# Kernel optimization log

Hardware: AMD Instinct MI355X
Metric: run time of the kernel (lower is better)

## Reference

```python
import jax, jax.numpy as jnp
import numpy as np

D_MODEL = 512
N_HEADS = 4
D_HEAD = D_MODEL // N_HEADS
D_FF = 2048
N_LAYERS = 3
IN_DIM = 25
OUT_DIM = 1
PRE = 20          # pre_training_size
SCALE = 10.0      # scaling_factor
EPS = 1e-5


def setup_inputs() -> dict:
    key = jax.random.key(0)
    ks = jax.random.split(key, 20)
    B, S = 4, 2048
    def gn(k, shape, fan_in):
        return jax.random.normal(k, shape, jnp.float32) * (1.0 / np.sqrt(fan_in))
    return {
        "src": jax.random.normal(ks[0], (B, S, IN_DIM), jnp.float32),
        "emb_w": gn(ks[1], (D_MODEL, IN_DIM), IN_DIM),
        "emb_b": jnp.zeros((D_MODEL,), jnp.float32),
        "in_w": gn(ks[2], (N_LAYERS, 3 * D_MODEL, D_MODEL), D_MODEL),
        "in_b": jnp.zeros((N_LAYERS, 3 * D_MODEL), jnp.float32),
        "out_w": gn(ks[3], (N_LAYERS, D_MODEL, D_MODEL), D_MODEL),
        "out_b": jnp.zeros((N_LAYERS, D_MODEL), jnp.float32),
        "ln1_g": jnp.ones((N_LAYERS, D_MODEL), jnp.float32),
        "ln1_b": jnp.zeros((N_LAYERS, D_MODEL), jnp.float32),
        "ln2_g": jnp.ones((N_LAYERS, D_MODEL), jnp.float32),
        "ln2_b": jnp.zeros((N_LAYERS, D_MODEL), jnp.float32),
        "ff1_w": gn(ks[4], (N_LAYERS, D_FF, D_MODEL), D_MODEL),
        "ff1_b": jnp.zeros((N_LAYERS, D_FF), jnp.float32),
        "ff2_w": gn(ks[5], (N_LAYERS, D_MODEL, D_FF), D_FF),
        "ff2_b": jnp.zeros((N_LAYERS, D_MODEL), jnp.float32),
        "dec_w": gn(ks[6], (OUT_DIM, D_MODEL), D_MODEL),
        "dec_b": jnp.zeros((OUT_DIM,), jnp.float32),
    }


def _layer_norm(x, g, b):
    mu = jnp.mean(x, axis=-1, keepdims=True)
    var = jnp.var(x, axis=-1, keepdims=True)
    return (x - mu) * jax.lax.rsqrt(var + EPS) * g + b


def _pos_encoding(seq_len):
    # eval mode: start index 0, no dropout
    pos = jnp.arange(seq_len, dtype=jnp.float32)[:, None]           # [S,1]
    div = jnp.exp(jnp.arange(0, D_MODEL, 2, dtype=jnp.float32) * (-np.log(10000.0) / D_MODEL))  # [D/2]
    ang = pos * div                                                  # [S,D/2]
    return jnp.stack([jnp.sin(ang), jnp.cos(ang)], axis=-1).reshape(seq_len, D_MODEL)


def _causal_mask(seq_len):
    row = jnp.arange(seq_len)[:, None]
    col = jnp.arange(seq_len)[None, :]
    mask = jnp.where(col <= row, 0.0, -jnp.inf).astype(jnp.float32)
    # include_training_period=True: first PRE x PRE block unmasked
    return mask.at[:PRE, :PRE].set(0.0)


def reference(src, emb_w, emb_b, in_w, in_b, out_w, out_b,
              ln1_g, ln1_b, ln2_g, ln2_b, ff1_w, ff1_b, ff2_w, ff2_b,
              dec_w, dec_b):
    B, S, _ = src.shape
    x = src @ emb_w.T + emb_b                    # [B,S,D]
    x = x + _pos_encoding(S)[None]
    mask = _causal_mask(S)                       # [S,S]
    scale = 1.0 / np.sqrt(D_HEAD)
    for l in range(N_LAYERS):
        # --- self-attention (post-norm, eager bmm+softmax+bmm path) ---
        qkv = x @ in_w[l].T + in_b[l]            # [B,S,3D]
        q, k, v = jnp.split(qkv, 3, axis=-1)
        q = q.reshape(B, S, N_HEADS, D_HEAD).transpose(0, 2, 1, 3)
        k = k.reshape(B, S, N_HEADS, D_HEAD).transpose(0, 2, 1, 3)
        v = v.reshape(B, S, N_HEADS, D_HEAD).transpose(0, 2, 1, 3)
        scores = jnp.einsum('bhqd,bhkd->bhqk', q, k) * scale + mask
        attn = jax.nn.softmax(scores, axis=-1)   # [B,H,S,S] (need_weights=True path)
        o = jnp.einsum('bhqk,bhkd->bhqd', attn, v)
        o = o.transpose(0, 2, 1, 3).reshape(B, S, D_MODEL)
        o = o @ out_w[l].T + out_b[l]
        x = _layer_norm(x + o, ln1_g[l], ln1_b[l])
        # --- FFN ---
        h = jax.nn.relu(x @ ff1_w[l].T + ff1_b[l])
        h = h @ ff2_w[l].T + ff2_b[l]
        x = _layer_norm(x + h, ln2_g[l], ln2_b[l])
    out = jnp.tanh(x @ dec_w.T + dec_b) * SCALE  # [B,S,1]
    return out
```

## Files before the change

kernel.cpp:

```cpp
#include <hip/hip_runtime.h>

#define S_LEN 2048
#define DMODEL 512

typedef __attribute__((ext_vector_type(8))) short bf16x8;
typedef __attribute__((ext_vector_type(4))) float f32x4;
typedef __attribute__((ext_vector_type(4))) unsigned short u16x4;
typedef __attribute__((ext_vector_type(8))) unsigned short u16x8;
typedef __attribute__((ext_vector_type(2))) unsigned int u32x2;

__device__ __forceinline__ unsigned short f2bf(float f) {
    unsigned int u = __float_as_uint(f);
    u += 0x7fff + ((u >> 16) & 1);
    return (unsigned short)(u >> 16);
}
__device__ __forceinline__ float bf2f(unsigned short h) {
    return __uint_as_float(((unsigned int)h) << 16);
}
__device__ __forceinline__ void gll16(const void* g, void* l) {
    __builtin_amdgcn_global_load_lds(
        (const __attribute__((address_space(1))) unsigned int*)g,
        (__attribute__((address_space(3))) unsigned int*)l, 16, 0, 0);
}

__global__ __launch_bounds__(256) void conv_all(
    const float4* __restrict__ in_w, const float4* __restrict__ out_w,
    const float4* __restrict__ ff1_w, const float4* __restrict__ ff2_w,
    u16x4* __restrict__ in_wb, u16x4* __restrict__ out_wb,
    u16x4* __restrict__ ff1_wb, u16x4* __restrict__ ff2_wb)
{
    int i = blockIdx.x * 256 + threadIdx.x;
    const float4* src; u16x4* dst; int j;
    if (i < 589824)        { src = in_w;  dst = in_wb;  j = i; }
    else if (i < 786432)   { src = out_w; dst = out_wb; j = i - 589824; }
    else if (i < 1572864)  { src = ff1_w; dst = ff1_wb; j = i - 786432; }
    else                   { src = ff2_w; dst = ff2_wb; j = i - 1572864; }
    float4 v = src[j];
    u16x4 o = { f2bf(v.x), f2bf(v.y), f2bf(v.z), f2bf(v.w) };
    dst[j] = o;
}

__global__ __launch_bounds__(256) void embed_kernel(
    const float* __restrict__ src, const float* __restrict__ ew,
    const float* __restrict__ eb, float* __restrict__ X,
    unsigned short* __restrict__ Xb)
{
    int rid = blockIdx.x;
    int s = rid & (S_LEN - 1);
    int tid = threadIdx.x;
    __shared__ float sr[25];
    if (tid < 25) sr[tid] = src[rid * 25 + tid];
    __syncthreads();
    #pragma unroll
    for (int rep = 0; rep < 2; rep++) {
        int d = tid + rep * 256;
        float a = eb[d];
        #pragma unroll
        for (int k = 0; k < 25; k++) a = fmaf(sr[k], ew[d * 25 + k], a);
        int i2 = d & ~1;
        float div = expf(-(float)i2 * (9.210340371976184f / 512.f));
        float ang = (float)s * div;
        a += (d & 1) ? cosf(ang) : sinf(ang);
        X[(size_t)rid * DMODEL + d] = a;
        Xb[(size_t)rid * DMODEL + d] = f2bf(a);
    }
}

template<int MODE, int BN>
__global__ __launch_bounds__(256) void gemm_bf16(
    const unsigned short* __restrict__ A, int lda,
    const unsigned short* __restrict__ W, int K,
    const float* __restrict__ bias,
    unsigned short* __restrict__ out, int ldc,
    unsigned short* __restrict__ out2)
{
    constexpr int NJ = BN / 32;
    __shared__ __align__(16) unsigned short As[2][128 * 64];
    __shared__ __align__(16) unsigned short Ws[2][BN * 64];
    int tid = threadIdx.x;
    int lane = tid & 63, w = tid >> 6;
    int g = lane >> 4, c15 = lane & 15;
    int wm = w >> 1, wn = w & 1;
    int bm, bn;
    if (BN == 64) {
        int raw = blockIdx.x;
        int lid = ((raw & 7) << 6) | (raw >> 3);
        bn = lid & 7; bm = lid >> 3;
    } else {
        bm = blockIdx.y; bn = blockIdx.x;
    }

    f32x4 acc[4][NJ];
    #pragma unroll
    for (int i = 0; i < 4; i++)
        #pragma unroll
        for (int j = 0; j < NJ; j++) acc[i][j] = (f32x4){0.f, 0.f, 0.f, 0.f};

    auto stage = [&](int kk, int bi) {
        #pragma unroll
        for (int i = 0; i < 4; i++) {
            int chunk = tid + i * 256;
            int r = chunk >> 3, c = chunk & 7;
            int cs = c ^ (r & 7);
            gll16(A + (size_t)(bm * 128 + r) * lda + kk * 64 + cs * 8,
                  (void*)(As[bi] + chunk * 8));
        }
        #pragma unroll
        for (int i = 0; i < BN / 32; i++) {
            int chunk = tid + i * 256;
            int r = chunk >> 3, c = chunk & 7;
            int cs = c ^ (r & 7);
            gll16(W + (size_t)(bn * BN + r) * K + kk * 64 + cs * 8,
                  (void*)(Ws[bi] + chunk * 8));
        }
    };

    const int nk = K >> 6;
    stage(0, 0);
    __syncthreads();
    int buf = 0;

    for (int kk = 0; kk < nk; kk++) {
        if (kk + 1 < nk) stage(kk + 1, buf ^ 1);
        bf16x8 a[4][2], b[NJ][2];
        #pragma unroll
        for (int mi = 0; mi < 4; mi++) {
            int row = wm * 64 + mi * 16 + c15;
            #pragma unroll
            for (int h = 0; h < 2; h++) {
                int ck = (h * 4 + g) ^ (row & 7);
                a[mi][h] = *(const bf16x8*)((const char*)As[buf] + row * 128 + ck * 16);
            }
        }
        #pragma unroll
        for (int nj = 0; nj < NJ; nj++) {
            int row = wn * (BN / 2) + nj * 16 + c15;
            #pragma unroll
            for (int h = 0; h < 2; h++) {
                int ck = (h * 4 + g) ^ (row & 7);
                b[nj][h] = *(const bf16x8*)((const char*)Ws[buf] + row * 128 + ck * 16);
            }
        }
        __builtin_amdgcn_s_setprio(1);
        #pragma unroll
        for (int h = 0; h < 2; h++)
            #pragma unroll
            for (int mi = 0; mi < 4; mi++)
                #pragma unroll
                for (int nj = 0; nj < NJ; nj++)
                    acc[mi][nj] = __builtin_amdgcn_mfma_f32_16x16x32_bf16(
                        a[mi][h], b[nj][h], acc[mi][nj], 0, 0, 0);
        __builtin_amdgcn_s_setprio(0);
        __syncthreads();
        buf ^= 1;
    }
    #pragma unroll
    for (int nj = 0; nj < NJ; nj++) {
        int colb = bn * BN + wn * (BN / 2) + nj * 16;
        float bv = bias[colb + c15];
        #pragma unroll
        for (int mi = 0; mi < 4; mi++) {
            int rowb = bm * 128 + wm * 64 + mi * 16 + g * 4;
            if (MODE == 3 && colb >= 1024) {
                int cv = colb - 1024 + c15;
                int hh = cv >> 7, d = cv & 127;
                int bb = rowb >> 11, t = rowb & (S_LEN - 1);
                u16x4 pk;
                #pragma unroll
                for (int r = 0; r < 4; r++) pk[r] = f2bf(acc[mi][nj][r] + bv);
                *(u16x4*)(out2 + ((size_t)(bb * 4 + hh) * 128 + d) * S_LEN + t) = pk;
            } else {
                #pragma unroll
                for (int r = 0; r < 4; r++) {
                    float v = acc[mi][nj][r] + bv;
                    if (MODE == 2) v = fmaxf(v, 0.f);
                    out[(size_t)(rowb + r) * ldc + colb + c15] = f2bf(v);
                }
            }
        }
    }
}

__global__ __launch_bounds__(256) void flash_attn(
    const unsigned short* __restrict__ QKb,
    const unsigned short* __restrict__ Vt,
    unsigned short* __restrict__ Ob,
    unsigned short* __restrict__ Opart,
    float* __restrict__ Mpart,
    float* __restrict__ Lpart)
{
    __shared__ __align__(16) unsigned short Ks[2][32 * 128];
    __shared__ __align__(16) unsigned short Vts[2][128 * 32];
    __shared__ __align__(16) unsigned short Plds[4][16 * 40];
    const float scale = 0.08838834764831845f;
    int tid = threadIdx.x;
    int lane = tid & 63, w = tid >> 6;
    int g = lane >> 4, c15 = lane & 15;
    int raw = blockIdx.x;
    int lid = (raw & 7) * 96 + (raw >> 3);
    int bh = lid / 48, idx = lid - bh * 48;
    int b = bh >> 2, h = bh & 3;
    int qb, kt0, nkt, split;
    if (idx < 16) { qb = idx; kt0 = 0; nkt = 2 * qb + 2; split = -1; }
    else {
        int s = idx - 16;
        qb = 16 + (s >> 1);
        int j = s & 1;
        kt0 = j * (qb + 1);
        nkt = qb + 1;
        split = bh * 32 + (qb - 16) * 2 + j;
    }

    bf16x8 q[4];
    {
        const unsigned short* qrow =
            QKb + (size_t)(b * S_LEN + qb * 64 + w * 16 + c15) * 1024 + h * 128;
        #pragma unroll
        for (int k0 = 0; k0 < 4; k0++) q[k0] = *(const bf16x8*)(qrow + k0 * 32 + g * 8);
    }
    f32x4 o[8];
    #pragma unroll
    for (int cd = 0; cd < 8; cd++) o[cd] = (f32x4){0.f, 0.f, 0.f, 0.f};
    float m = -3e38f, l = 0.f;

    auto stage = [&](int kt, int bi) {
        #pragma unroll
        for (int i = 0; i < 2; i++) {
            int chunk = tid + i * 256;
            int r = chunk >> 4, c = chunk & 15;
            int cs = (c & 8) | ((c ^ r) & 7);
            gll16(QKb + (size_t)(b * S_LEN + kt * 32 + r) * 1024 + 512 + h * 128 + cs * 8,
                  (void*)(Ks[bi] + chunk * 8));
        }
        #pragma unroll
        for (int i = 0; i < 2; i++) {
            int chunk = tid + i * 256;
            int r = chunk >> 2, c = chunk & 3;
            int cs = (c ^ r) & 3;
            gll16(Vt + ((size_t)(b * 4 + h) * 128 + r) * S_LEN + kt * 32 + cs * 8,
                  (void*)(Vts[bi] + chunk * 8));
        }
    };

    stage(kt0, 0);
    __syncthreads();
    int buf = 0;

    for (int t = 0; t < nkt; t++) {
        int kt = kt0 + t;
        if (t + 1 < nkt) stage(kt + 1, buf ^ 1);
        f32x4 sf[2];
        __builtin_amdgcn_s_setprio(1);
        #pragma unroll
        for (int c = 0; c < 2; c++) {
            sf[c] = (f32x4){0.f, 0.f, 0.f, 0.f};
            int tok16 = c * 16 + c15;
            #pragma unroll
            for (int k0 = 0; k0 < 4; k0++) {
                int ck = k0 * 4 + g;
                int cs = (ck & 8) | ((ck ^ tok16) & 7);
                bf16x8 kf = *(const bf16x8*)((const char*)Ks[buf] + tok16 * 256 + cs * 16);
                sf[c] = __builtin_amdgcn_mfma_f32_16x16x32_bf16(kf, q[k0], sf[c], 0, 0, 0);
            }
        }
        __builtin_amdgcn_s_setprio(0);
        if (kt >= 2 * qb) {
            int qr = qb * 64 + w * 16 + c15;
            #pragma unroll
            for (int c = 0; c < 2; c++)
                #pragma unroll
                for (int r = 0; r < 4; r++) {
                    int tok = kt * 32 + c * 16 + g * 4 + r;
                    bool ok = (tok <= qr) || (qr < 20 && tok < 20);
                    if (!ok) sf[c][r] = -3e38f;
                }
        }
        float t0 = fmaxf(fmaxf(sf[0][0], sf[0][1]), fmaxf(sf[0][2], sf[0][3]));
        float t1 = fmaxf(fmaxf(sf[1][0], sf[1][1]), fmaxf(sf[1][2], sf[1][3]));
        float mt = fmaxf(t0, t1);
        mt = fmaxf(mt, __shfl_xor(mt, 16));
        mt = fmaxf(mt, __shfl_xor(mt, 32));
        bool need = !__all(mt <= m + 90.5f);
        float sc = 1.f;
        if (need) {
            float mn = fmaxf(m, mt);
            sc = __expf((m - mn) * scale);
            m = mn;
        }
        float msc = m * scale;
        #pragma unroll
        for (int c = 0; c < 2; c++)
            #pragma unroll
            for (int r = 0; r < 4; r++)
                sf[c][r] = __expf(fmaf(sf[c][r], scale, -msc));
        float s0 = (sf[0][0] + sf[0][1]) + (sf[0][2] + sf[0][3]);
        float s1 = (sf[1][0] + sf[1][1]) + (sf[1][2] + sf[1][3]);
        float ls = s0 + s1;
        ls += __shfl_xor(ls, 16);
        ls += __shfl_xor(ls, 32);
        if (need) l *= sc;
        l += ls;
        #pragma unroll
        for (int c = 0; c < 2; c++) {
            unsigned int lo = ((unsigned int)f2bf(sf[c][1]) << 16) | f2bf(sf[c][0]);
            unsigned int hi = ((unsigned int)f2bf(sf[c][3]) << 16) | f2bf(sf[c][2]);
            u32x2 pk = {lo, hi};
            *(u32x2*)&Plds[w][c15 * 40 + c * 16 + g * 4] = pk;
        }
        if (need) {
            float r0 = __shfl(sc, g * 4 + 0);
            float r1 = __shfl(sc, g * 4 + 1);
            float r2 = __shfl(sc, g * 4 + 2);
            float r3 = __shfl(sc, g * 4 + 3);
            #pragma unroll
            for (int cd = 0; cd < 8; cd++) {
                o[cd][0] *= r0; o[cd][1] *= r1; o[cd][2] *= r2; o[cd][3] *= r3;
            }
        }
        bf16x8 pa = *(const bf16x8*)((const char*)&Plds[w][0] + c15 * 80 + g * 16);
        __builtin_amdgcn_s_setprio(1);
        #pragma unroll
        for (int cd = 0; cd < 8; cd++) {
            int dv = cd * 16 + c15;
            int cs = (g ^ dv) & 3;
            bf16x8 vf = *(const bf16x8*)((const char*)Vts[buf] + dv * 64 + cs * 16);
            o[cd] = __builtin_amdgcn_mfma_f32_16x16x32_bf16(pa, vf, o[cd], 0, 0, 0);
        }
        __builtin_amdgcn_s_setprio(0);
        __syncthreads();
        buf ^= 1;
    }

    if (split < 0) {
        float li0 = 1.f / __shfl(l, g * 4 + 0);
        float li1 = 1.f / __shfl(l, g * 4 + 1);
        float li2 = 1.f / __shfl(l, g * 4 + 2);
        float li3 = 1.f / __shfl(l, g * 4 + 3);
        size_t obase = (size_t)(b * S_LEN + qb * 64 + w * 16 + g * 4) * 512 + h * 128;
        #pragma unroll
        for (int cd = 0; cd < 8; cd++) {
            Ob[obase + 0 * 512 + cd * 16 + c15] = f2bf(o[cd][0] * li0);
            Ob[obase + 1 * 512 + cd * 16 + c15] = f2bf(o[cd][1] * li1);
            Ob[obase + 2 * 512 + cd * 16 + c15] = f2bf(o[cd][2] * li2);
            Ob[obase + 3 * 512 + cd * 16 + c15] = f2bf(o[cd][3] * li3);
        }
    } else {
        unsigned short* op = Opart + (size_t)split * 8192;
        int rb = w * 16 + g * 4;
        #pragma unroll
        for (int cd = 0; cd < 8; cd++) {
            op[(rb + 0) * 128 + cd * 16 + c15] = f2bf(o[cd][0]);
            op[(rb + 1) * 128 + cd * 16 + c15] = f2bf(o[cd][1]);
            op[(rb + 2) * 128 + cd * 16 + c15] = f2bf(o[cd][2]);
            op[(rb + 3) * 128 + cd * 16 + c15] = f2bf(o[cd][3]);
        }
        if (g == 0) {
            Mpart[split * 64 + w * 16 + c15] = m;
            Lpart[split * 64 + w * 16 + c15] = l;
        }
    }
}

__global__ __launch_bounds__(256) void attn_merge(
    const unsigned short* __restrict__ Opart,
    const float* __restrict__ Mpart, const float* __restrict__ Lpart,
    unsigned short* __restrict__ Ob)
{
    const float scale = 0.08838834764831845f;
    int bid = blockIdx.x;
    int bh = bid >> 4, qe = bid & 15;
    int qb = 16 + qe;
    int b = bh >> 2, h = bh & 3;
    int p0 = bh * 32 + qe * 2;
    int t = threadIdx.x;
    int r = t >> 2, dq = t & 3;
    float m0 = Mpart[p0 * 64 + r], m1 = Mpart[(p0 + 1) * 64 + r];
    float l0 = Lpart[p0 * 64 + r], l1 = Lpart[(p0 + 1) * 64 + r];
    float ms = fmaxf(m0, m1);
    float w0 = __expf((m0 - ms) * scale), w1 = __expf((m1 - ms) * scale);
    float linv = 1.f / (l0 * w0 + l1 * w1);
    w0 *= linv; w1 *= linv;
    const unsigned short* o0 = Opart + (size_t)p0 * 8192 + r * 128 + dq * 32;
    const unsigned short* o1 = o0 + 8192;
    unsigned short* od = Ob + (size_t)(b * S_LEN + qb * 64 + r) * 512 + h * 128 + dq * 32;
    #pragma unroll
    for (int i = 0; i < 4; i++) {
        u16x8 a = *(const u16x8*)(o0 + i * 8);
        u16x8 c = *(const u16x8*)(o1 + i * 8);
        u16x8 d;
        #pragma unroll
        for (int j = 0; j < 8; j++)
            d[j] = f2bf(bf2f(a[j]) * w0 + bf2f(c[j]) * w1);
        *(u16x8*)(od + i * 8) = d;
    }
}

__global__ __launch_bounds__(256) void add_ln_kernel(
    float* __restrict__ X, const unsigned short* __restrict__ D,
    const float* __restrict__ gw, const float* __restrict__ bw,
    unsigned short* __restrict__ Xb)
{
    int wv = threadIdx.x >> 6, lane = threadIdx.x & 63;
    int row = blockIdx.x * 4 + wv;
    size_t base = (size_t)row * DMODEL + lane * 8;
    float4 x0 = *(const float4*)(X + base);
    float4 x1 = *(const float4*)(X + base + 4);
    u16x8 d8 = *(const u16x8*)(D + base);
    float v[8];
    v[0] = x0.x + bf2f(d8[0]); v[1] = x0.y + bf2f(d8[1]);
    v[2] = x0.z + bf2f(d8[2]); v[3] = x0.w + bf2f(d8[3]);
    v[4] = x1.x + bf2f(d8[4]); v[5] = x1.y + bf2f(d8[5]);
    v[6] = x1.z + bf2f(d8[6]); v[7] = x1.w + bf2f(d8[7]);
    float s = 0.f, sq = 0.f;
    #pragma unroll
    for (int i = 0; i < 8; i++) { s += v[i]; sq = fmaf(v[i], v[i], sq); }
    #pragma unroll
    for (int off = 32; off > 0; off >>= 1) {
        s  += __shfl_xor(s, off);
        sq += __shfl_xor(sq, off);
    }
    float mu = s * (1.f / DMODEL);
    float var = sq * (1.f / DMODEL) - mu * mu;
    float rs = rsqrtf(var + 1e-5f);
    float4 g0 = *(const float4*)(gw + lane * 8);
    float4 g1 = *(const float4*)(gw + lane * 8 + 4);
    float4 b0 = *(const float4*)(bw + lane * 8);
    float4 b1 = *(const float4*)(bw + lane * 8 + 4);
    float y[8];
    y[0] = (v[0] - mu) * rs * g0.x + b0.x; y[1] = (v[1] - mu) * rs * g0.y + b0.y;
    y[2] = (v[2] - mu) * rs * g0.z + b0.z; y[3] = (v[3] - mu) * rs * g0.w + b0.w;
    y[4] = (v[4] - mu) * rs * g1.x + b1.x; y[5] = (v[5] - mu) * rs * g1.y + b1.y;
    y[6] = (v[6] - mu) * rs * g1.z + b1.z; y[7] = (v[7] - mu) * rs * g1.w + b1.w;
    float4 o0 = { y[0], y[1], y[2], y[3] };
    float4 o1 = { y[4], y[5], y[6], y[7] };
    *(float4*)(X + base) = o0;
    *(float4*)(X + base + 4) = o1;
    u16x8 ob;
    #pragma unroll
    for (int i = 0; i < 8; i++) ob[i] = f2bf(y[i]);
    *(u16x8*)(Xb + base) = ob;
}

__global__ __launch_bounds__(256) void decoder_kernel(
    const float* __restrict__ X, const float* __restrict__ w,
    const float* __restrict__ bias, float* __restrict__ out)
{
    int tid = threadIdx.x;
    int lane = tid & 63;
    int row = blockIdx.x * 4 + (tid >> 6);
    float s = 0.f;
    size_t base = (size_t)row * DMODEL;
    #pragma unroll
    for (int i = 0; i < 8; i++) s = fmaf(X[base + lane + i * 64], w[lane + i * 64], s);
    #pragma unroll
    for (int off = 32; off > 0; off >>= 1) s += __shfl_down(s, off);
    if (lane == 0) out[row] = tanhf(s + bias[0]) * 10.0f;
}

extern "C" void kernel_launch(void* const* d_in, const int* in_sizes, int n_in,
                              void* d_out, int out_size, void* d_ws, size_t ws_size,
                              hipStream_t stream)
{
    const float* src   = (const float*)d_in[0];
    const float* emb_w = (const float*)d_in[1];
    const float* emb_b = (const float*)d_in[2];
    const float* in_w  = (const float*)d_in[3];
    const float* in_b  = (const float*)d_in[4];
    const float* out_w = (const float*)d_in[5];
    const float* out_b = (const float*)d_in[6];
    const float* ln1_g = (const float*)d_in[7];
    const float* ln1_b = (const float*)d_in[8];
    const float* ln2_g = (const float*)d_in[9];
    const float* ln2_b = (const float*)d_in[10];
    const float* ff1_w = (const float*)d_in[11];
    const float* ff1_b = (const float*)d_in[12];
    const float* ff2_w = (const float*)d_in[13];
    const float* ff2_b = (const float*)d_in[14];
    const float* dec_w = (const float*)d_in[15];
    const float* dec_b = (const float*)d_in[16];

    char* ws = (char*)d_ws;
    float*          X   = (float*)ws;
    unsigned short* Xb  = (unsigned short*)(ws + (16u << 20));
    unsigned short* Pb  = (unsigned short*)(ws + (24u << 20));
    unsigned short* Ob  = (unsigned short*)(ws + (32u << 20));
    unsigned short* QKb = (unsigned short*)(ws + (40u << 20));
    unsigned short* Vt  = (unsigned short*)(ws + (56u << 20));
    unsigned short* Hb  = (unsigned short*)(ws + (40u << 20));
    unsigned short* Opart = (unsigned short*)(ws + (16u << 20));
    float* Mpart = (float*)(ws + (24u << 20));
    float* Lpart = Mpart + 512 * 64;
    unsigned short* in_wb  = (unsigned short*)(ws + (72u << 20));
    unsigned short* out_wb = in_wb  + 3u * 1536 * 512;
    unsigned short* ff1_wb = out_wb + 3u * 512 * 512;
    unsigned short* ff2_wb = ff1_wb + 3u * 2048 * 512;
    float* outp = (float*)d_out;
    const int M = 4 * S_LEN;

    conv_all<<<9216, 256, 0, stream>>>(
        (const float4*)in_w, (const float4*)out_w,
        (const float4*)ff1_w, (const float4*)ff2_w,
        (u16x4*)in_wb, (u16x4*)out_wb, (u16x4*)ff1_wb, (u16x4*)ff2_wb);

    embed_kernel<<<M, 256, 0, stream>>>(src, emb_w, emb_b, X, Xb);

    for (int l = 0; l < 3; l++) {
        gemm_bf16<3, 128><<<dim3(12, 64), 256, 0, stream>>>(
            Xb, 512, in_wb + (size_t)l * 1536 * 512, 512, in_b + l * 1536,
            QKb, 1024, Vt);
        flash_attn<<<768, 256, 0, stream>>>(QKb, Vt, Ob, Opart, Mpart, Lpart);
        attn_merge<<<256, 256, 0, stream>>>(Opart, Mpart, Lpart, Ob);
        gemm_bf16<1, 64><<<dim3(512), 256, 0, stream>>>(
            Ob, 512, out_wb + (size_t)l * 512 * 512, 512, out_b + l * 512,
            Pb, 512, nullptr);
        add_ln_kernel<<<M / 4, 256, 0, stream>>>(X, Pb, ln1_g + l * 512, ln1_b + l * 512, Xb);
        gemm_bf16<2, 128><<<dim3(16, 64), 256, 0, stream>>>(
            Xb, 512, ff1_wb + (size_t)l * 2048 * 512, 512, ff1_b + l * 2048,
            Hb, 2048, nullptr);
        gemm_bf16<1, 64><<<dim3(512), 256, 0, stream>>>(
            Hb, 2048, ff2_wb + (size_t)l * 512 * 2048, 2048, ff2_b + l * 512,
            Pb, 512, nullptr);
        add_ln_kernel<<<M / 4, 256, 0, stream>>>(X, Pb, ln2_g + l * 512, ln2_b + l * 512, Xb);
    }

    decoder_kernel<<<M / 4, 256, 0, stream>>>(X, dec_w, dec_b, outp);
}
```

Measured before the change: 538.8 us.

## Stage GEMM epilogue through LDS for vectorized stores and remap block order

```diff
diff --git a/kernel.cpp b/kernel.cpp
--- a/kernel.cpp
+++ b/kernel.cpp
@@ -72,11 +72,11 @@
     const unsigned short* __restrict__ W, int K,
     const float* __restrict__ bias,
     unsigned short* __restrict__ out, int ldc,
-    unsigned short* __restrict__ out2)
+    unsigned short* __restrict__ out2, int nbn)
 {
     constexpr int NJ = BN / 32;
-    __shared__ __align__(16) unsigned short As[2][128 * 64];
-    __shared__ __align__(16) unsigned short Ws[2][BN * 64];
+    constexpr int WC = BN / 2;
+    __shared__ __align__(16) unsigned short LdsBuf[2][(128 + BN) * 64];
     int tid = threadIdx.x;
     int lane = tid & 63, w = tid >> 6;
     int g = lane >> 4, c15 = lane & 15;
@@ -87,7 +87,10 @@
         int lid = ((raw & 7) << 6) | (raw >> 3);
         bn = lid & 7; bm = lid >> 3;
     } else {
-        bm = blockIdx.y; bn = blockIdx.x;
+        int raw = blockIdx.x;
+        int per = gridDim.x >> 3;
+        int lid = (raw & 7) * per + (raw >> 3);
+        bn = lid % nbn; bm = lid / nbn;
     }
 
     f32x4 acc[4][NJ];
@@ -103,7 +106,7 @@
             int r = chunk >> 3, c = chunk & 7;
             int cs = c ^ (r & 7);
             gll16(A + (size_t)(bm * 128 + r) * lda + kk * 64 + cs * 8,
-                  (void*)(As[bi] + chunk * 8));
+                  (void*)(LdsBuf[bi] + chunk * 8));
         }
         #pragma unroll
         for (int i = 0; i < BN / 32; i++) {
@@ -111,7 +114,7 @@
             int r = chunk >> 3, c = chunk & 7;
             int cs = c ^ (r & 7);
             gll16(W + (size_t)(bn * BN + r) * K + kk * 64 + cs * 8,
-                  (void*)(Ws[bi] + chunk * 8));
+                  (void*)(LdsBuf[bi] + 128 * 64 + chunk * 8));
         }
     };
 
@@ -129,16 +132,17 @@
             #pragma unroll
             for (int h = 0; h < 2; h++) {
                 int ck = (h * 4 + g) ^ (row & 7);
-                a[mi][h] = *(const bf16x8*)((const char*)As[buf] + row * 128 + ck * 16);
+                a[mi][h] = *(const bf16x8*)((const char*)LdsBuf[buf] + row * 128 + ck * 16);
             }
         }
         #pragma unroll
         for (int nj = 0; nj < NJ; nj++) {
-            int row = wn * (BN / 2) + nj * 16 + c15;
+            int row = wn * WC + nj * 16 + c15;
             #pragma unroll
             for (int h = 0; h < 2; h++) {
                 int ck = (h * 4 + g) ^ (row & 7);
-                b[nj][h] = *(const bf16x8*)((const char*)Ws[buf] + row * 128 + ck * 16);
+                b[nj][h] = *(const bf16x8*)((const char*)(LdsBuf[buf] + 128 * 64)
+                                            + row * 128 + ck * 16);
             }
         }
         __builtin_amdgcn_s_setprio(1);
@@ -154,29 +158,49 @@
         __syncthreads();
         buf ^= 1;
     }
+
+    unsigned short* scr = (unsigned short*)LdsBuf + (size_t)w * 4608;
+    int colb0 = bn * BN + wn * WC;
+    int rowb0 = bm * 128 + wm * 64;
+    bool vout = (MODE == 3) && (colb0 >= 1024);
     #pragma unroll
     for (int nj = 0; nj < NJ; nj++) {
-        int colb = bn * BN + wn * (BN / 2) + nj * 16;
-        float bv = bias[colb + c15];
+        float bv = bias[colb0 + nj * 16 + c15];
         #pragma unroll
         for (int mi = 0; mi < 4; mi++) {
-            int rowb = bm * 128 + wm * 64 + mi * 16 + g * 4;
-            if (MODE == 3 && colb >= 1024) {
-                int cv = colb - 1024 + c15;
-                int hh = cv >> 7, d = cv & 127;
-                int bb = rowb >> 11, t = rowb & (S_LEN - 1);
-                u16x4 pk;
-                #pragma unroll
-                for (int r = 0; r < 4; r++) pk[r] = f2bf(acc[mi][nj][r] + bv);
-                *(u16x4*)(out2 + ((size_t)(bb * 4 + hh) * 128 + d) * S_LEN + t) = pk;
-            } else {
-                #pragma unroll
-                for (int r = 0; r < 4; r++) {
-                    float v = acc[mi][nj][r] + bv;
-                    if (MODE == 2) v = fmaxf(v, 0.f);
-                    out[(size_t)(rowb + r) * ldc + colb + c15] = f2bf(v);
-                }
+            #pragma unroll
+            for (int r = 0; r < 4; r++) {
+                float v = acc[mi][nj][r] + bv;
+                if (MODE == 2) v = fmaxf(v, 0.f);
+                int rl = mi * 16 + g * 4 + r;
+                int cl = nj * 16 + c15;
+                if (!vout) scr[rl * 72 + cl] = f2bf(v);
+                else       scr[cl * 72 + rl] = f2bf(v);
             }
+        }
+    }
+    constexpr int NP = WC / 8;
+    if (!vout) {
+        #pragma unroll
+        for (int p = 0; p < NP; p++) {
+            int idx = p * 64 + lane;
+            int row = idx / (WC / 8);
+            int cc  = (idx % (WC / 8)) * 8;
+            u16x8 v = *(const u16x8*)(scr + row * 72 + cc);
+            *(u16x8*)(out + (size_t)(rowb0 + row) * ldc + colb0 + cc) = v;
+        }
+    } else {
+        int cv0 = colb0 - 1024;
+        int hh = cv0 >> 7, d0 = cv0 & 127;
+        int bb = rowb0 >> 11, t0 = rowb0 & (S_LEN - 1);
+        unsigned short* vbase = out2 + ((size_t)(bb * 4 + hh) * 128 + d0) * S_LEN + t0;
+        #pragma unroll
+        for (int p = 0; p < 8; p++) {
+            int idx = p * 64 + lane;
+            int rd = idx >> 3;
+            int tc = (idx & 7) * 8;
+            u16x8 v = *(const u16x8*)(scr + rd * 72 + tc);
+            *(u16x8*)(vbase + (size_t)rd * S_LEN + tc) = v;
         }
     }
 }
@@ -505,21 +529,21 @@
     embed_kernel<<<M, 256, 0, stream>>>(src, emb_w, emb_b, X, Xb);
 
     for (int l = 0; l < 3; l++) {
-        gemm_bf16<3, 128><<<dim3(12, 64), 256, 0, stream>>>(
+        gemm_bf16<3, 128><<<dim3(768), 256, 0, stream>>>(
             Xb, 512, in_wb + (size_t)l * 1536 * 512, 512, in_b + l * 1536,
-            QKb, 1024, Vt);
+            QKb, 1024, Vt, 12);
         flash_attn<<<768, 256, 0, stream>>>(QKb, Vt, Ob, Opart, Mpart, Lpart);
         attn_merge<<<256, 256, 0, stream>>>(Opart, Mpart, Lpart, Ob);
         gemm_bf16<1, 64><<<dim3(512), 256, 0, stream>>>(
             Ob, 512, out_wb + (size_t)l * 512 * 512, 512, out_b + l * 512,
-            Pb, 512, nullptr);
+            Pb, 512, nullptr, 8);
         add_ln_kernel<<<M / 4, 256, 0, stream>>>(X, Pb, ln1_g + l * 512, ln1_b + l * 512, Xb);
-        gemm_bf16<2, 128><<<dim3(16, 64), 256, 0, stream>>>(
+        gemm_bf16<2, 128><<<dim3(1024), 256, 0, stream>>>(
             Xb, 512, ff1_wb + (size_t)l * 2048 * 512, 512, ff1_b + l * 2048,
-            Hb, 2048, nullptr);
+            Hb, 2048, nullptr, 16);
         gemm_bf16<1, 64><<<dim3(512), 256, 0, stream>>>(
             Hb, 2048, ff2_wb + (size_t)l * 512 * 2048, 2048, ff2_b + l * 512,
-            Pb, 512, nullptr);
+            Pb, 512, nullptr, 8);
         add_ln_kernel<<<M / 4, 256, 0, stream>>>(X, Pb, ln2_g + l * 512, ln2_b + l * 512, Xb);
     }
 
```

New measurement: 517.0 us. 1.04x faster.
